# Optimization experiments

Hardware: AMD Instinct MI355X
Metric: run time of the kernel (lower is better)

## Reference

```python
import jax, jax.numpy as jnp
import numpy as np

B, SWIN_D, VIT_D, E, H = 16384, 768, 512, 1024, 4
HD = E // H  # 256


def setup_inputs() -> dict:
    key = jax.random.key(0)
    ks = jax.random.split(key, 12)
    s = lambda fan_in: 1.0 / np.sqrt(fan_in)
    return {
        "swin_feat": jax.random.normal(ks[0], (B, SWIN_D), jnp.float32),
        "vit_feat": jax.random.normal(ks[1], (B, VIT_D), jnp.float32),
        # outer projections (nn.Linear: y = x @ W.T + b)
        "Wq": jax.random.uniform(ks[2], (E, SWIN_D), jnp.float32, -s(SWIN_D), s(SWIN_D)),
        "bq": jax.random.uniform(ks[3], (E,), jnp.float32, -s(SWIN_D), s(SWIN_D)),
        "Wk": jax.random.uniform(ks[4], (E, VIT_D), jnp.float32, -s(VIT_D), s(VIT_D)),
        "bk": jax.random.uniform(ks[5], (E,), jnp.float32, -s(VIT_D), s(VIT_D)),
        "Wv": jax.random.uniform(ks[6], (E, VIT_D), jnp.float32, -s(VIT_D), s(VIT_D)),
        "bv": jax.random.uniform(ks[7], (E,), jnp.float32, -s(VIT_D), s(VIT_D)),
        # nn.MultiheadAttention internal in_proj (stacked q,k,v) and out_proj
        "in_proj_w": jax.random.uniform(ks[8], (3 * E, E), jnp.float32, -s(E), s(E)),
        "in_proj_b": jnp.zeros((3 * E,), jnp.float32),
        "Wo": jax.random.uniform(ks[9], (E, E), jnp.float32, -s(E), s(E)),
        "bo": jnp.zeros((E,), jnp.float32),
    }


def reference(swin_feat, vit_feat, Wq, bq, Wk, bk, Wv, bv, in_proj_w, in_proj_b, Wo, bo):
    # outer projections -> [B, E] (seq_len = 1, so the seq dim is implicit)
    q = swin_feat @ Wq.T + bq
    k = vit_feat @ Wk.T + bk
    v = vit_feat @ Wv.T + bv
    # MultiheadAttention in-projection (split stacked weight)
    Wiq, Wik, Wiv = in_proj_w[:E], in_proj_w[E:2 * E], in_proj_w[2 * E:]
    biq, bik, biv = in_proj_b[:E], in_proj_b[E:2 * E], in_proj_b[2 * E:]
    q2 = (q @ Wiq.T + biq).reshape(B, H, HD)
    k2 = (k @ Wik.T + bik).reshape(B, H, HD)
    v2 = (v @ Wiv.T + biv).reshape(B, H, HD)
    # attention with q_len = kv_len = 1
    scale = 1.0 / np.sqrt(HD)
    scores = jnp.einsum('bhd,bhd->bh', q2, k2) * scale        # [B, H]
    w = jax.nn.softmax(scores[..., None], axis=-1)             # softmax over 1 key -> ones
    attn = w * v2                                              # [B, H, HD]
    out = attn.reshape(B, E) @ Wo.T + bo                       # out-projection
    return out
```

## Files before the change

kernel.cpp:

```cpp
#include <hip/hip_runtime.h>
#include <stdint.h>
#include <stddef.h>

#define E_DIM 1024

typedef __bf16 v8bf __attribute__((ext_vector_type(8)));
typedef float v4f __attribute__((ext_vector_type(4)));

__device__ __forceinline__ unsigned short f2bf(float x) {
  unsigned int u = __builtin_bit_cast(unsigned int, x);
  u += 0x7fffu + ((u >> 16) & 1u);
  return (unsigned short)(u >> 16);
}

template <int RB>
__device__ __forceinline__ int swz(int r, int c) {
  if constexpr (RB >= 128) return c ^ ((r & 7) << 4);
  else return c;
}

template <int N>
__device__ __forceinline__ void waitcnt_vm() {
  static_assert(N == 0 || N == 4 || N == 8 || N == 12, "add literal");
  if constexpr (N == 0)  asm volatile("s_waitcnt vmcnt(0)" ::: "memory");
  if constexpr (N == 4)  asm volatile("s_waitcnt vmcnt(4)" ::: "memory");
  if constexpr (N == 8)  asm volatile("s_waitcnt vmcnt(8)" ::: "memory");
  if constexpr (N == 12) asm volatile("s_waitcnt vmcnt(12)" ::: "memory");
}

template <int ROWS, int BK>
__device__ __forceinline__ void stageg(const unsigned short* __restrict__ G, int g0,
                                       int ldg, int k0, char* L, int wid, int lane) {
  constexpr int RB = BK * 2;
  constexpr int ITERS = (ROWS * RB) / 4096;
#pragma unroll
  for (int it = 0; it < ITERS; ++it) {
    int lbase = it * 4096 + wid * 1024;
    int lin = lbase + lane * 16;
    int r = lin / RB, cb = lin % RB;
    int gcb = swz<RB>(r, cb);
    const char* g = (const char*)G + ((size_t)(g0 + r) * ldg + k0) * 2 + gcb;
    __builtin_amdgcn_global_load_lds((const __attribute__((address_space(1))) void*)g,
                                     (__attribute__((address_space(3))) void*)(L + lbase),
                                     16, 0, 0);
  }
}

template <int RB>
__device__ __forceinline__ v8bf frag_bf16(const char* L, int r, int kelem) {
  int o = swz<RB>(r, kelem * 2);
  return *(const v8bf*)(L + r * RB + o);
}

template <int BM, int BN, int BK, int FM, int FN>
__device__ __forceinline__ void compute_tile(const char* Al, const char* Bl,
                                             v4f (&acc)[FM][FN],
                                             int wr, int wc, int lr, int kg) {
  constexpr int RBA = BK * 2, RBB = BK * 2;
  constexpr int TMW = BM / 2, TNW = BN / 2;
#pragma unroll
  for (int kk = 0; kk < BK / 32; ++kk) {
    const int ke = kk * 32 + kg * 8;
    v8bf a[FM], b[FN];
#pragma unroll
    for (int mi = 0; mi < FM; ++mi)
      a[mi] = frag_bf16<RBA>(Al, wr * TMW + mi * 16 + lr, ke);
#pragma unroll
    for (int ni = 0; ni < FN; ++ni)
      b[ni] = frag_bf16<RBB>(Bl, wc * TNW + ni * 16 + lr, ke);
#pragma unroll
    for (int mi = 0; mi < FM; ++mi)
#pragma unroll
      for (int ni = 0; ni < FN; ++ni)
        acc[mi][ni] = __builtin_amdgcn_mfma_f32_16x16x32_bf16(a[mi], b[ni], acc[mi][ni], 0, 0, 0);
  }
}

__device__ __forceinline__ void cvt4(const float4* __restrict__ src,
                                     ushort4* __restrict__ dst, int i0) {
#pragma unroll
  for (int j = 0; j < 4; ++j) {
    int i = i0 + j * 256;
    float4 f = src[i];
    ushort4 u;
    u.x = f2bf(f.x); u.y = f2bf(f.y); u.z = f2bf(f.z); u.w = f2bf(f.w);
    dst[i] = u;
  }
}

__global__ __launch_bounds__(256) void prep1(const float* __restrict__ Wv,
                                             unsigned short* __restrict__ WvT,
                                             const float* __restrict__ Wiv,
                                             const float* __restrict__ bv,
                                             const float* __restrict__ biv,
                                             float* __restrict__ b1,
                                             const float* __restrict__ vit,
                                             unsigned short* __restrict__ Xb,
                                             unsigned short* __restrict__ Wivb,
                                             const float* __restrict__ Wo,
                                             unsigned short* __restrict__ Wob) {
  int bid = blockIdx.x;
  int tid = threadIdx.x;
  if (bid < 512) {
    __shared__ float tile[32][33];
    const int R = 1024, C = 512;
    int nbx = C >> 5;
    int bx = bid % nbx, by = bid / nbx;
    int tx = tid & 31, ty = tid >> 5;
#pragma unroll
    for (int i = 0; i < 32; i += 8)
      tile[ty + i][tx] = Wv[(size_t)(by * 32 + ty + i) * C + bx * 32 + tx];
    __syncthreads();
#pragma unroll
    for (int i = 0; i < 32; i += 8)
      WvT[(size_t)(bx * 32 + ty + i) * R + by * 32 + tx] = f2bf(tile[tx][ty + i]);
  } else if (bid < 768) {
    int r = (bid - 512) * 4 + (tid >> 6);
    int lane = tid & 63;
    float s = 0.f;
    for (int c = lane; c < 1024; c += 64) s += Wiv[(size_t)r * 1024 + c] * bv[c];
#pragma unroll
    for (int off = 32; off; off >>= 1) s += __shfl_down(s, off);
    if (lane == 0) b1[r] = s + biv[r];
  } else if (bid < 2816) {
    cvt4((const float4*)vit, (ushort4*)Xb, (bid - 768) * 1024 + tid);
  } else if (bid < 3072) {
    cvt4((const float4*)Wiv, (ushort4*)Wivb, (bid - 2816) * 1024 + tid);
  } else {
    cvt4((const float4*)Wo, (ushort4*)Wob, (bid - 3072) * 1024 + tid);
  }
}

template <int BM, int BN, int BK, int FM, int FN, int OUTBF, int XCDSWZ>
__global__ __launch_bounds__(256) void gemm_cv(const unsigned short* __restrict__ A,
                                               const unsigned short* __restrict__ B,
                                               const float* __restrict__ bias,
                                               float* __restrict__ Cf,
                                               unsigned short* __restrict__ Cb,
                                               int M, int N, int K,
                                               const float* __restrict__ mvW,
                                               const float* __restrict__ mvx,
                                               const float* __restrict__ mvb,
                                               float* __restrict__ mvy) {
  static_assert((BM + BN) * BK * 2 / 1024 / 4 == 4, "vmcnt literals assume 4 loads/tile/wave");
  __shared__ __align__(16) char Al0[BM * BK * 2];
  __shared__ __align__(16) char Al1[BM * BK * 2];
  __shared__ __align__(16) char Al2[BM * BK * 2];
  __shared__ __align__(16) char Al3[BM * BK * 2];
  __shared__ __align__(16) char Bl0[BN * BK * 2];
  __shared__ __align__(16) char Bl1[BN * BK * 2];
  __shared__ __align__(16) char Bl2[BN * BK * 2];
  __shared__ __align__(16) char Bl3[BN * BK * 2];
  const int nbn = N / BN;
  const int ngemm = nbn * (M / BM);
  int bid = blockIdx.x;
  const int tid = threadIdx.x;

  if (bid >= ngemm) {
    int r = (bid - ngemm) * 4 + (tid >> 6);
    int lane = tid & 63;
    float s = 0.f;
    for (int c = lane; c < 1024; c += 64) s += mvW[(size_t)r * 1024 + c] * mvx[c];
#pragma unroll
    for (int off = 32; off; off >>= 1) s += __shfl_down(s, off);
    if (lane == 0) mvy[r] = s + mvb[r];
    return;
  }

  int bm_i, bn_i;
  if (XCDSWZ) {
    int x = bid & 7, j = bid >> 3;
    bm_i = x + ((j >> 3) << 3);
    bn_i = j & 7;
  } else {
    bm_i = bid / nbn;
    bn_i = bid % nbn;
  }
  const int bm0 = bm_i * BM, bn0 = bn_i * BN;

  constexpr int TMW = BM / 2, TNW = BN / 2;
  const int lane = tid & 63;
  const int wid = tid >> 6;
  const int wr = wid >> 1, wc = wid & 1;
  const int lr = lane & 15;
  const int kg = lane >> 4;

  v4f acc[FM][FN];
#pragma unroll
  for (int i = 0; i < FM; ++i)
#pragma unroll
    for (int j = 0; j < FN; ++j) acc[i][j] = 0.f;

  const int NT = K / BK;

  stageg<BM, BK>(A, bm0, K, 0 * BK, Al0, wid, lane);
  stageg<BN, BK>(B, bn0, K, 0 * BK, Bl0, wid, lane);
  stageg<BM, BK>(A, bm0, K, 1 * BK, Al1, wid, lane);
  stageg<BN, BK>(B, bn0, K, 1 * BK, Bl1, wid, lane);
  stageg<BM, BK>(A, bm0, K, 2 * BK, Al2, wid, lane);
  stageg<BN, BK>(B, bn0, K, 2 * BK, Bl2, wid, lane);
  stageg<BM, BK>(A, bm0, K, 3 * BK, Al3, wid, lane);
  stageg<BN, BK>(B, bn0, K, 3 * BK, Bl3, wid, lane);

#define GEMM_PHASE(AB, BB, TNXT, W)                                      \
  waitcnt_vm<W>();                                                       \
  __builtin_amdgcn_s_barrier();                                          \
  __builtin_amdgcn_sched_barrier(0);                                     \
  compute_tile<BM, BN, BK, FM, FN>(AB, BB, acc, wr, wc, lr, kg);         \
  __builtin_amdgcn_sched_barrier(0);                                     \
  asm volatile("s_waitcnt lgkmcnt(0)" ::: "memory");                     \
  __builtin_amdgcn_s_barrier();                                          \
  if ((TNXT) < NT) {                                                     \
    stageg<BM, BK>(A, bm0, K, (TNXT)*BK, AB, wid, lane);                 \
    stageg<BN, BK>(B, bn0, K, (TNXT)*BK, BB, wid, lane);                 \
  }

  for (int t = 0; t < NT - 4; t += 4) {
    GEMM_PHASE(Al0, Bl0, t + 4, 12)
    GEMM_PHASE(Al1, Bl1, t + 5, 12)
    GEMM_PHASE(Al2, Bl2, t + 6, 12)
    GEMM_PHASE(Al3, Bl3, t + 7, 12)
  }
  GEMM_PHASE(Al0, Bl0, NT, 12)
  GEMM_PHASE(Al1, Bl1, NT, 8)
  GEMM_PHASE(Al2, Bl2, NT, 4)
  GEMM_PHASE(Al3, Bl3, NT, 0)
#undef GEMM_PHASE

#pragma unroll
  for (int ni = 0; ni < FN; ++ni) {
    int col = bn0 + wc * TNW + ni * 16 + lr;
    float bz = bias ? bias[col] : 0.f;
#pragma unroll
    for (int mi = 0; mi < FM; ++mi) {
      int row0 = bm0 + wr * TMW + mi * 16 + kg * 4;
#pragma unroll
      for (int r = 0; r < 4; ++r) {
        float v = acc[mi][ni][r] + bz;
        if (OUTBF) Cb[(size_t)(row0 + r) * N + col] = f2bf(v);
        else       Cf[(size_t)(row0 + r) * N + col] = v;
      }
    }
  }
}

extern "C" void kernel_launch(void* const* d_in, const int* in_sizes, int n_in,
                              void* d_out, int out_size, void* d_ws, size_t ws_size,
                              hipStream_t stream) {
  const float* vit = (const float*)d_in[1];
  const float* Wv  = (const float*)d_in[6];
  const float* bv  = (const float*)d_in[7];
  const float* ipw = (const float*)d_in[8];
  const float* ipb = (const float*)d_in[9];
  const float* Wo  = (const float*)d_in[10];
  const float* bo  = (const float*)d_in[11];
  const float* Wiv = ipw + 2 * E_DIM * E_DIM;
  const float* biv = ipb + 2 * E_DIM;

  char* ws = (char*)d_ws;
  unsigned short* Xb   = (unsigned short*)(ws);
  unsigned short* Wivb = (unsigned short*)(ws + (16 << 20));
  unsigned short* Wob  = (unsigned short*)(ws + (18 << 20));
  unsigned short* WvTb = (unsigned short*)(ws + (20 << 20));
  unsigned short* Ttb  = (unsigned short*)(ws + (21 << 20));
  unsigned short* Wcb  = (unsigned short*)(ws + (22 << 20));
  float* b1 = (float*)(ws + (23 << 20));
  float* bc = (float*)(ws + (23 << 20) + 4096);

  prep1<<<3328, 256, 0, stream>>>(Wv, WvTb, Wiv, bv, biv, b1, vit, Xb, Wivb, Wo, Wob);

  gemm_cv<64, 64, 64, 2, 2, 1, 0><<<128 + 256, 256, 0, stream>>>(
      WvTb, Wivb, nullptr, nullptr, Ttb, 512, 1024, 1024, Wo, b1, bo, bc);

  gemm_cv<64, 64, 64, 2, 2, 1, 0><<<128, 256, 0, stream>>>(
      Wob, Ttb, nullptr, nullptr, Wcb, 1024, 512, 1024,
      nullptr, nullptr, nullptr, nullptr);

  gemm_cv<128, 128, 32, 4, 4, 0, 1><<<1024, 256, 0, stream>>>(
      Xb, Wcb, bc, (float*)d_out, nullptr, 16384, 1024, 512,
      nullptr, nullptr, nullptr, nullptr);
}
```

Measured before the change: 59.64 us.

## Distribute input conversion work across small GEMM launches to overlap with them

Moves the fp32-to-bf16 conversion of vit_feat and Wo out of the prep kernel and into the extra blocks of the two small weight-folding GEMM launches, split across both. The conversions now run alongside under-occupied small GEMMs (128 tiles each) rather than serially before them. The cost is larger grids and more branching in the GEMM kernel. Each conversion's output must also be finished before the kernel that consumes it.

Measured after the change: 59.94 us. No clear change (+0.5%).

```diff
diff --git a/kernel.cpp b/kernel.cpp
--- a/kernel.cpp
+++ b/kernel.cpp
@@ -88,17 +88,25 @@
   }
 }
 
+__device__ __forceinline__ void mv4(const float* __restrict__ W, const float* __restrict__ x,
+                                    const float* __restrict__ b, float* __restrict__ y,
+                                    int blkrel, int tid) {
+  int r = blkrel * 4 + (tid >> 6);
+  int lane = tid & 63;
+  float s = 0.f;
+  for (int c = lane; c < 1024; c += 64) s += W[(size_t)r * 1024 + c] * x[c];
+#pragma unroll
+  for (int off = 32; off; off >>= 1) s += __shfl_down(s, off);
+  if (lane == 0) y[r] = s + b[r];
+}
+
 __global__ __launch_bounds__(256) void prep1(const float* __restrict__ Wv,
                                              unsigned short* __restrict__ WvT,
                                              const float* __restrict__ Wiv,
                                              const float* __restrict__ bv,
                                              const float* __restrict__ biv,
                                              float* __restrict__ b1,
-                                             const float* __restrict__ vit,
-                                             unsigned short* __restrict__ Xb,
-                                             unsigned short* __restrict__ Wivb,
-                                             const float* __restrict__ Wo,
-                                             unsigned short* __restrict__ Wob) {
+                                             unsigned short* __restrict__ Wivb) {
   int bid = blockIdx.x;
   int tid = threadIdx.x;
   if (bid < 512) {
@@ -115,19 +123,9 @@
     for (int i = 0; i < 32; i += 8)
       WvT[(size_t)(bx * 32 + ty + i) * R + by * 32 + tx] = f2bf(tile[tx][ty + i]);
   } else if (bid < 768) {
-    int r = (bid - 512) * 4 + (tid >> 6);
-    int lane = tid & 63;
-    float s = 0.f;
-    for (int c = lane; c < 1024; c += 64) s += Wiv[(size_t)r * 1024 + c] * bv[c];
-#pragma unroll
-    for (int off = 32; off; off >>= 1) s += __shfl_down(s, off);
-    if (lane == 0) b1[r] = s + biv[r];
-  } else if (bid < 2816) {
-    cvt4((const float4*)vit, (ushort4*)Xb, (bid - 768) * 1024 + tid);
-  } else if (bid < 3072) {
-    cvt4((const float4*)Wiv, (ushort4*)Wivb, (bid - 2816) * 1024 + tid);
+    mv4(Wiv, bv, biv, b1, bid - 512, tid);
   } else {
-    cvt4((const float4*)Wo, (ushort4*)Wob, (bid - 3072) * 1024 + tid);
+    cvt4((const float4*)Wiv, (ushort4*)Wivb, (bid - 768) * 1024 + tid);
   }
 }
 
@@ -141,7 +139,13 @@
                                                const float* __restrict__ mvW,
                                                const float* __restrict__ mvx,
                                                const float* __restrict__ mvb,
-                                               float* __restrict__ mvy) {
+                                               float* __restrict__ mvy, int nmv,
+                                               const float* __restrict__ csrc1,
+                                               unsigned short* __restrict__ cdst1,
+                                               int cbase1, int ncv1,
+                                               const float* __restrict__ csrc2,
+                                               unsigned short* __restrict__ cdst2,
+                                               int cbase2) {
   static_assert((BM + BN) * BK * 2 / 1024 / 4 == 4, "vmcnt literals assume 4 loads/tile/wave");
   __shared__ __align__(16) char Al0[BM * BK * 2];
   __shared__ __align__(16) char Al1[BM * BK * 2];
@@ -157,13 +161,14 @@
   const int tid = threadIdx.x;
 
   if (bid >= ngemm) {
-    int r = (bid - ngemm) * 4 + (tid >> 6);
-    int lane = tid & 63;
-    float s = 0.f;
-    for (int c = lane; c < 1024; c += 64) s += mvW[(size_t)r * 1024 + c] * mvx[c];
-#pragma unroll
-    for (int off = 32; off; off >>= 1) s += __shfl_down(s, off);
-    if (lane == 0) mvy[r] = s + mvb[r];
+    int rel = bid - ngemm;
+    if (rel < nmv) {
+      mv4(mvW, mvx, mvb, mvy, rel, tid);
+    } else if (rel < nmv + ncv1) {
+      cvt4((const float4*)csrc1, (ushort4*)cdst1, (cbase1 + rel - nmv) * 1024 + tid);
+    } else {
+      cvt4((const float4*)csrc2, (ushort4*)cdst2, (cbase2 + rel - nmv - ncv1) * 1024 + tid);
+    }
     return;
   }
 
@@ -267,16 +272,23 @@
   float* b1 = (float*)(ws + (23 << 20));
   float* bc = (float*)(ws + (23 << 20) + 4096);
 
-  prep1<<<3328, 256, 0, stream>>>(Wv, WvTb, Wiv, bv, biv, b1, vit, Xb, Wivb, Wo, Wob);
-
-  gemm_cv<64, 64, 64, 2, 2, 1, 0><<<128 + 256, 256, 0, stream>>>(
-      WvTb, Wivb, nullptr, nullptr, Ttb, 512, 1024, 1024, Wo, b1, bo, bc);
-
-  gemm_cv<64, 64, 64, 2, 2, 1, 0><<<128, 256, 0, stream>>>(
+  prep1<<<1024, 256, 0, stream>>>(Wv, WvTb, Wiv, bv, biv, b1, Wivb);
+
+  gemm_cv<64, 64, 64, 2, 2, 1, 0><<<128 + 256 + 256 + 1024, 256, 0, stream>>>(
+      WvTb, Wivb, nullptr, nullptr, Ttb, 512, 1024, 1024,
+      Wo, b1, bo, bc, 256,
+      Wo, Wob, 0, 256,
+      vit, Xb, 0);
+
+  gemm_cv<64, 64, 64, 2, 2, 1, 0><<<128 + 1024, 256, 0, stream>>>(
       Wob, Ttb, nullptr, nullptr, Wcb, 1024, 512, 1024,
-      nullptr, nullptr, nullptr, nullptr);
+      nullptr, nullptr, nullptr, nullptr, 0,
+      vit, Xb, 1024, 1024,
+      vit, Xb, 0);
 
   gemm_cv<128, 128, 32, 4, 4, 0, 1><<<1024, 256, 0, stream>>>(
       Xb, Wcb, bc, (float*)d_out, nullptr, 16384, 1024, 512,
-      nullptr, nullptr, nullptr, nullptr);
-}
+      nullptr, nullptr, nullptr, nullptr, 0,
+      nullptr, nullptr, 0, 0,
+      nullptr, nullptr, 0);
+}
```
